# Performance work log

Hardware: AMD Instinct MI355X
Metric: run time of the kernel (lower is better)

## Reference

```python
import jax, jax.numpy as jnp
import numpy as np

B, S, P, D, H, L, DFF = 4, 2048, 32, 512, 8, 2, 2048
HD = D // H
NV = 8  # number of variates; S = NV * 256 patches
SCALE = 1.0 / np.sqrt(HD)


def _rope_tables(seq_len, dim, base=10000.0):
    inv = 1.0 / (base ** (jnp.arange(0, dim, 2, dtype=jnp.float32) / dim))
    freqs = jnp.outer(jnp.arange(seq_len, dtype=jnp.float32), inv)  # (S, dim/2)
    emb = jnp.concatenate([freqs, freqs], axis=-1)  # (S, dim)
    return jnp.cos(emb), jnp.sin(emb)


def _apply_rope(x, cos, sin):
    # x: (..., S, HD); cos/sin: (S, HD)
    x1, x2 = x[..., ::2], x[..., 1::2]
    ch, sh = cos[..., ::2], sin[..., ::2]
    r1 = x1 * ch - x2 * sh
    r2 = x1 * sh + x2 * ch
    return jnp.stack([r1, r2], axis=-1).reshape(x.shape)


def _ln(x, g, b, eps=1e-5):
    m = x.mean(-1, keepdims=True)
    v = x.var(-1, keepdims=True)
    return (x - m) / jnp.sqrt(v + eps) * g + b


def setup_inputs() -> dict:
    key = jax.random.key(0)
    ks = jax.random.split(key, 20)
    s = 0.02
    x = jax.random.normal(ks[0], (B, S, P), dtype=jnp.float32)
    # 8 variates, 256 patches each, flattened: [0]*256, [1]*256, ...
    variate_ids = jnp.broadcast_to(jnp.arange(S, dtype=jnp.int32) // (S // NV), (B, S))
    mask = jnp.ones((B, S), dtype=jnp.float32)
    f32 = jnp.float32
    return {
        'x': x, 'variate_ids': variate_ids, 'mask': mask,
        'W_pe': jax.random.normal(ks[1], (P, D), f32) * s, 'b_pe': jnp.zeros((D,), f32),
        'Wq': jax.random.normal(ks[2], (L, D, D), f32) * s, 'bq': jnp.zeros((L, D), f32),
        'Wk': jax.random.normal(ks[3], (L, D, D), f32) * s, 'bk': jnp.zeros((L, D), f32),
        'Wv': jax.random.normal(ks[4], (L, D, D), f32) * s, 'bv': jnp.zeros((L, D), f32),
        'Wo': jax.random.normal(ks[5], (L, D, D), f32) * s, 'bo': jnp.zeros((L, D), f32),
        'u_same': jax.random.normal(ks[6], (L, H), f32) * 0.1,
        'u_cross': jax.random.normal(ks[7], (L, H), f32) * 0.1,
        'g1': jnp.ones((L, D), f32), 'be1': jnp.zeros((L, D), f32),
        'W1': jax.random.normal(ks[8], (L, D, DFF), f32) * s, 'b1f': jnp.zeros((L, DFF), f32),
        'W2': jax.random.normal(ks[9], (L, DFF, D), f32) * s, 'b2f': jnp.zeros((L, D), f32),
        'g2': jnp.ones((L, D), f32), 'be2': jnp.zeros((L, D), f32),
        'Wh': jax.random.normal(ks[10], (D, P), f32) * s, 'bh': jnp.zeros((P,), f32),
    }


def reference(x, variate_ids, mask, W_pe, b_pe, Wq, bq, Wk, bk, Wv, bv, Wo, bo,
              u_same, u_cross, g1, be1, W1, b1f, W2, b2f, g2, be2, Wh, bh):
    b, s, _ = x.shape
    h = x @ W_pe + b_pe  # patch embedding: (B,S,D)
    cos, sin = _rope_tables(s, HD)
    same = (variate_ids[:, :, None] == variate_ids[:, None, :]).astype(h.dtype)  # (B,S,S)
    mask_add = (1.0 - mask)[:, None, None, :] * -1e9  # (B,1,1,S)
    for l in range(L):
        q = (h @ Wq[l] + bq[l]).reshape(b, s, H, HD).transpose(0, 2, 1, 3)
        k = (h @ Wk[l] + bk[l]).reshape(b, s, H, HD).transpose(0, 2, 1, 3)
        v = (h @ Wv[l] + bv[l]).reshape(b, s, H, HD).transpose(0, 2, 1, 3)
        q = _apply_rope(q, cos, sin)
        k = _apply_rope(k, cos, sin)
        scores = jnp.einsum('bhqd,bhkd->bhqk', q, k) * SCALE
        bias = (same[:, None] * u_same[l][None, :, None, None]
                + (1.0 - same)[:, None] * u_cross[l][None, :, None, None])
        scores = scores + bias + mask_add
        p = jax.nn.softmax(scores, axis=-1)
        o = jnp.einsum('bhqk,bhkd->bhqd', p, v).transpose(0, 2, 1, 3).reshape(b, s, D)
        o = o @ Wo[l] + bo[l]
        h = _ln(h + o, g1[l], be1[l])
        f = jax.nn.gelu(h @ W1[l] + b1f[l], approximate=False) @ W2[l] + b2f[l]
        h = _ln(h + f, g2[l], be2[l])
    return h @ Wh + bh  # forecasting head: (B,S,P)
```

## Files before the change

kernel.cpp:

```cpp
#include <hip/hip_runtime.h>

typedef unsigned short u16;
typedef unsigned int   u32;
typedef __attribute__((ext_vector_type(8))) short bf16x8;
typedef __attribute__((ext_vector_type(4))) short bf16x4;
typedef __attribute__((ext_vector_type(4))) float f32x4;
typedef __attribute__((ext_vector_type(4))) int   i32x4;

constexpr int B_ = 4, S_ = 2048, D_ = 512, H_ = 8, L_ = 2, DFF_ = 2048;
constexpr int BS_ = B_ * S_;
constexpr float QSC_ = 0.18033688011f;
constexpr float LOG2E_ = 1.44269504089f;

__device__ __forceinline__ u16 f2bf(float f) {
    u32 u = __float_as_uint(f);
    u += 0x7fffu + ((u >> 16) & 1u);
    return (u16)(u >> 16);
}
__device__ __forceinline__ float bf2f(u16 u) {
    return __uint_as_float(((u32)u) << 16);
}
__device__ __forceinline__ u32 cvt_pk_bf16(float lo, float hi) {
    u32 d;
    asm volatile("v_cvt_pk_bf16_f32 %0, %1, %2" : "=v"(d) : "v"(lo), "v"(hi));
    return d;
}
__device__ __forceinline__ float exp2v(float x) {
    float d;
    asm("v_exp_f32 %0, %1" : "=v"(d) : "v"(x));
    return d;
}

__global__ __launch_bounds__(256)
void wtrans_all(const float* __restrict__ Wpe, const float* __restrict__ Wq,
                const float* __restrict__ Wk, const float* __restrict__ Wv,
                const float* __restrict__ Wo, const float* __restrict__ W1,
                const float* __restrict__ W2, u16* __restrict__ wpe_t,
                u16* __restrict__ wbase)
{
    __shared__ float tile[32][33];
    int id = blockIdx.x;
    const float* src; u16* dst; int K, N, tx, ty;
    if (id < 16) {
        src = Wpe; dst = wpe_t; K = 32; N = 512; tx = id; ty = 0;
    } else {
        id -= 16;
        if (id < 2048) {
            int mat = id >> 8, l = mat >> 2, w = mat & 3;
            const float* srcs[4] = { Wq, Wk, Wv, Wo };
            src = srcs[w] + (size_t)l * 262144;
            u16* base = wbase + (size_t)l * 3145728;
            dst = base + (size_t)w * 262144;
            K = 512; N = 512;
            int t8 = id & 255; tx = t8 & 15; ty = t8 >> 4;
        } else if (id < 4096) {
            id -= 2048;
            int l = id >> 10, t = id & 1023;
            src = W1 + (size_t)l * 1048576;
            dst = wbase + (size_t)l * 3145728 + 1048576;
            K = 512; N = 2048; tx = t & 63; ty = t >> 6;
        } else {
            id -= 4096;
            int l = id >> 10, t = id & 1023;
            src = W2 + (size_t)l * 1048576;
            dst = wbase + (size_t)l * 3145728 + 2097152;
            K = 2048; N = 512; tx = t & 15; ty = t >> 4;
        }
    }
    const int n0 = tx * 32, k0 = ty * 32;
    const int t = threadIdx.x;
#pragma unroll
    for (int i = 0; i < 4; i++) {
        int lin = i * 256 + t;
        int r = lin >> 5, c = lin & 31;
        tile[r][c] = src[(size_t)(k0 + r) * N + n0 + c];
    }
    __syncthreads();
#pragma unroll
    for (int i = 0; i < 4; i++) {
        int lin = i * 256 + t;
        int r = lin >> 5, c = lin & 31;
        dst[(size_t)(n0 + r) * K + k0 + c] = f2bf(tile[c][r]);
    }
}

__global__ __launch_bounds__(256)
void misc_prep(const float* __restrict__ x, u16* __restrict__ xb,
               const float* __restrict__ bq, const float* __restrict__ bk,
               const float* __restrict__ bv, float* __restrict__ bqkv,
               float* __restrict__ rc, float* __restrict__ rs)
{
    const int id = blockIdx.x, t = threadIdx.x;
    if (id < 256) {
        int idx = id * 256 + t;
        int j = idx & 31, tpos = idx >> 5;
        float inv = __expf(-(float)j * 0.28782313662425572f);
        float ang = (float)tpos * inv;
        rc[idx] = cosf(ang);
        rs[idx] = sinf(ang);
    } else if (id < 512) {
        int i = (id - 256) * 256 + t;
        float4 f = *reinterpret_cast<const float4*>(x + (size_t)i * 4);
        uint2 pk;
        pk.x = (u32)f2bf(f.x) | ((u32)f2bf(f.y) << 16);
        pk.y = (u32)f2bf(f.z) | ((u32)f2bf(f.w) << 16);
        *reinterpret_cast<uint2*>(xb + (size_t)i * 4) = pk;
    } else {
        int idx = (id - 512) * 256 + t;
        if (idx < L_ * 1536) {
            int l = idx / 1536, i = idx % 1536;
            float v = (i < 512) ? bq[l * 512 + i]
                    : (i < 1024) ? bk[l * 512 + i - 512]
                                 : bv[l * 512 + i - 1024];
            bqkv[idx] = v;
        }
    }
}

template<int ACT, int BN, int ROPE>
__global__ __launch_bounds__(256)
void gemm_kernel(const u16* __restrict__ A, const u16* __restrict__ Bt,
                 const float* __restrict__ bias, u16* __restrict__ C,
                 int M, int N, int K, int lda,
                 u16* __restrict__ qd, u16* __restrict__ kd, u16* __restrict__ vd,
                 const float* __restrict__ rc, const float* __restrict__ rs)
{
    constexpr int LDT = 40;
    constexpr int NI = BN / 32;
    __shared__ u16 As[128 * LDT];
    __shared__ u16 Bs[BN * LDT];
    const int t = threadIdx.x;
    const int m0 = blockIdx.y * 128, n0 = blockIdx.x * BN;
    const int lane = t & 63, w = t >> 6;
    const int wr = w >> 1, wc = w & 1;
    const int l15 = lane & 15, lhi = lane >> 4;

    f32x4 acc[4][NI];
#pragma unroll
    for (int i = 0; i < 4; i++)
#pragma unroll
        for (int j = 0; j < NI; j++)
#pragma unroll
            for (int r = 0; r < 4; r++) acc[i][j][r] = 0.f;

    for (int kt = 0; kt < K; kt += 32) {
#pragma unroll
        for (int i = 0; i < 2; i++) {
            int lin = i * 256 + t;
            int r = lin >> 2, c8 = (lin & 3) << 3;
            *reinterpret_cast<bf16x8*>(&As[r * LDT + c8]) =
                *reinterpret_cast<const bf16x8*>(A + (size_t)(m0 + r) * lda + kt + c8);
        }
#pragma unroll
        for (int i = 0; i < BN / 64; i++) {
            int lin = i * 256 + t;
            int r = lin >> 2, c8 = (lin & 3) << 3;
            *reinterpret_cast<bf16x8*>(&Bs[r * LDT + c8]) =
                *reinterpret_cast<const bf16x8*>(Bt + (size_t)(n0 + r) * K + kt + c8);
        }
        __syncthreads();
        bf16x8 af[4], bfv[NI];
#pragma unroll
        for (int mi = 0; mi < 4; mi++)
            af[mi] = *reinterpret_cast<const bf16x8*>(&As[(wr * 64 + mi * 16 + l15) * LDT + lhi * 8]);
#pragma unroll
        for (int ni = 0; ni < NI; ni++)
            bfv[ni] = *reinterpret_cast<const bf16x8*>(&Bs[(wc * (BN / 2) + ni * 16 + l15) * LDT + lhi * 8]);
#pragma unroll
        for (int mi = 0; mi < 4; mi++)
#pragma unroll
            for (int ni = 0; ni < NI; ni++)
                acc[mi][ni] = __builtin_amdgcn_mfma_f32_16x16x32_bf16(af[mi], bfv[ni], acc[mi][ni], 0, 0, 0);
        __syncthreads();
    }

    float bb[NI];
#pragma unroll
    for (int ni = 0; ni < NI; ni++) bb[ni] = bias[n0 + wc * (BN / 2) + ni * 16 + l15];
#pragma unroll
    for (int mi = 0; mi < 4; mi++) {
        int row = m0 + wr * 64 + mi * 16 + lhi * 4;
#pragma unroll
        for (int ni = 0; ni < NI; ni++) {
            int col = n0 + wc * (BN / 2) + ni * 16 + l15;
#pragma unroll
            for (int r = 0; r < 4; r++) {
                float v = acc[mi][ni][r] + bb[ni];
                if (ACT == 1) v = 0.5f * v * (1.0f + erff(v * 0.70710678118654752f));
                C[(size_t)(row + r) * N + col] = f2bf(v);
            }
        }
    }
}

template<int ACT, int BN, int ROPE>
__global__ __launch_bounds__(256)
void gemm_db(const u16* __restrict__ A, const u16* __restrict__ Bt,
             const float* __restrict__ bias, u16* __restrict__ C,
             int M, int N, int K, int lda,
             u16* __restrict__ qd, u16* __restrict__ kd, u16* __restrict__ vd,
             const float* __restrict__ rc, const float* __restrict__ rs)
{
    constexpr int NI = BN / 32;
    constexpr int ABYTES = 128 * 128;
    constexpr int BBYTES = BN * 128;
    constexpr int HALF = ABYTES + BBYTES;
    __shared__ char lds[2 * HALF];
    const int t = threadIdx.x;
    const int m0 = blockIdx.y * 128, n0 = blockIdx.x * BN;
    const int lane = t & 63, w = t >> 6;
    const int wr = w >> 1, wc = w & 1;
    const int l15 = lane & 15, lhi = lane >> 4;
    const int sw = (l15 & 7) << 4;

    auto stage = [&](int kt, int buf) {
        char* base = lds + buf * HALF;
#pragma unroll
        for (int p = 0; p < ABYTES / 4096; p++) {
            int off = p * 4096 + t * 16;
            int so = off ^ (((off >> 7) & 7) << 4);
            int row = off >> 7;
            int col = (so & 127) >> 1;
            __builtin_amdgcn_global_load_lds(
                (const __attribute__((address_space(1))) void*)(A + (size_t)(m0 + row) * lda + kt + col),
                (__attribute__((address_space(3))) void*)(base + off), 16, 0, 0);
        }
        char* bb = base + ABYTES;
#pragma unroll
        for (int p = 0; p < BBYTES / 4096; p++) {
            int off = p * 4096 + t * 16;
            int so = off ^ (((off >> 7) & 7) << 4);
            int row = off >> 7;
            int col = (so & 127) >> 1;
            __builtin_amdgcn_global_load_lds(
                (const __attribute__((address_space(1))) void*)(Bt + (size_t)(n0 + row) * K + kt + col),
                (__attribute__((address_space(3))) void*)(bb + off), 16, 0, 0);
        }
    };

    f32x4 acc[4][NI];
#pragma unroll
    for (int i = 0; i < 4; i++)
#pragma unroll
        for (int j = 0; j < NI; j++)
#pragma unroll
            for (int r = 0; r < 4; r++) acc[i][j][r] = 0.f;

    stage(0, 0);
    int buf = 0;
    for (int kt = 0; kt < K; kt += 64) {
        if (kt + 64 < K) {
            stage(kt + 64, buf ^ 1);
            if constexpr (BN == 64) asm volatile("s_waitcnt vmcnt(6)" ::: "memory");
            else                    asm volatile("s_waitcnt vmcnt(8)" ::: "memory");
        } else {
            asm volatile("s_waitcnt vmcnt(0)" ::: "memory");
        }
        __builtin_amdgcn_s_barrier();
        const char* La = lds + buf * HALF;
        const char* Lb = La + ABYTES;
        bf16x8 af[4][2], bfv[NI][2];
#pragma unroll
        for (int mi = 0; mi < 4; mi++) {
            int row = wr * 64 + mi * 16 + l15;
#pragma unroll
            for (int kk = 0; kk < 2; kk++)
                af[mi][kk] = *reinterpret_cast<const bf16x8*>(La + ((row * 128 + kk * 64 + lhi * 16) ^ sw));
        }
#pragma unroll
        for (int ni = 0; ni < NI; ni++) {
            int row = wc * (BN / 2) + ni * 16 + l15;
#pragma unroll
            for (int kk = 0; kk < 2; kk++)
                bfv[ni][kk] = *reinterpret_cast<const bf16x8*>(Lb + ((row * 128 + kk * 64 + lhi * 16) ^ sw));
        }
        __builtin_amdgcn_s_setprio(1);
#pragma unroll
        for (int kk = 0; kk < 2; kk++)
#pragma unroll
            for (int mi = 0; mi < 4; mi++)
#pragma unroll
                for (int ni = 0; ni < NI; ni++)
                    acc[mi][ni] = __builtin_amdgcn_mfma_f32_16x16x32_bf16(af[mi][kk], bfv[ni][kk], acc[mi][ni], 0, 0, 0);
        __builtin_amdgcn_s_setprio(0);
        __builtin_amdgcn_s_barrier();
        buf ^= 1;
    }

    float bb[NI];
#pragma unroll
    for (int ni = 0; ni < NI; ni++) bb[ni] = bias[n0 + wc * (BN / 2) + ni * 16 + l15];

    if (ROPE == 0) {
#pragma unroll
        for (int mi = 0; mi < 4; mi++) {
            int row = m0 + wr * 64 + mi * 16 + lhi * 4;
#pragma unroll
            for (int ni = 0; ni < NI; ni++) {
                int col = n0 + wc * (BN / 2) + ni * 16 + l15;
#pragma unroll
                for (int r = 0; r < 4; r++) {
                    float v = acc[mi][ni][r] + bb[ni];
                    if (ACT == 1) v = 0.5f * v * (1.0f + erff(v * 0.70710678118654752f));
                    C[(size_t)(row + r) * N + col] = f2bf(v);
                }
            }
        }
    } else {
#pragma unroll
        for (int ni = 0; ni < NI; ni++) {
            int colb = n0 + wc * (BN / 2) + ni * 16;
            int region = colb >> 9;
            int col = colb + l15;
            int d = col & 63;
            int head = (col >> 6) & 7;
#pragma unroll
            for (int mi = 0; mi < 4; mi++) {
                int row0 = m0 + wr * 64 + mi * 16 + lhi * 4;
                int sp0 = row0 & (S_ - 1);
                int bidx0 = row0 >> 11;
                if (region == 2) {
                    float vv[4];
#pragma unroll
                    for (int r = 0; r < 4; r++) vv[r] = acc[mi][ni][r] + bb[ni];
                    uint2 pk;
                    pk.x = (u32)f2bf(vv[0]) | ((u32)f2bf(vv[1]) << 16);
                    pk.y = (u32)f2bf(vv[2]) | ((u32)f2bf(vv[3]) << 16);
                    *reinterpret_cast<uint2*>(vd + (((size_t)(bidx0 * 8 + head) * 64 + d) << 11) + sp0) = pk;
                } else {
#pragma unroll
                    for (int r = 0; r < 4; r++) {
                        int sp = sp0 + r;
                        float v = acc[mi][ni][r] + bb[ni];
                        float px = __shfl_xor(v, 1);
                        int f = d & 30;
                        float cs = rc[sp * 32 + f], sn = rs[sp * 32 + f];
                        float ov = (l15 & 1) ? fmaf(px, sn, v * cs)
                                             : fmaf(v, cs, -(px * sn));
                        if (region == 0) ov *= QSC_;
                        u16* dst = (region == 0) ? qd : kd;
                        dst[((size_t)(bidx0 * 8 + head) * S_ + sp) * 64 + d] = f2bf(ov);
                    }
                }
            }
        }
    }
}

__global__ __launch_bounds__(512, 4)
void attn_kernel(const u16* __restrict__ qbp, const u16* __restrict__ kbp,
                 const u16* __restrict__ vt, const int* __restrict__ vid,
                 const float* __restrict__ maskp,
                 const float* __restrict__ usame, const float* __restrict__ ucross,
                 u16* __restrict__ o)
{
    __shared__ u16 ldsK[3][64 * 64];
    __shared__ u16 ldsV[3][64 * 64];
    __shared__ int   vids[S_];
    __shared__ float madds[S_];
    const int bidx = blockIdx.x;
    const int xcd = bidx & 7;
    const int j = bidx >> 3;
    const int bh = xcd * 4 + (j >> 4);
    const int chunk = j & 15;
    const int b = bh >> 3, hh = bh & 7;
    const int t = threadIdx.x;
    const int lane = t & 63, wid = t >> 6;
    const int q0 = chunk * 128 + wid * 16;
    const int l15 = lane & 15, lhi = lane >> 4;
    const int sw = (l15 & 7) << 4;
    const int ssw = ((t >> 3) & 7) << 4;
    const u16* qp = qbp + (size_t)bh * S_ * 64;
    const u16* kp = kbp + (size_t)bh * S_ * 64;
    const u16* vp = vt + (size_t)bh * 64 * S_;
    const float us = usame[hh] * LOG2E_, uc = ucross[hh] * LOG2E_;
    const int* vidb = vid + (size_t)b * S_;
    const float* mkb = maskp + (size_t)b * S_;
    const bf16x4 ones = { (short)0x3F80, (short)0x3F80, (short)0x3F80, (short)0x3F80 };

    bf16x8 qfr[2];
#pragma unroll
    for (int kk = 0; kk < 2; kk++)
        qfr[kk] = *reinterpret_cast<const bf16x8*>(
            qp + (size_t)(q0 + l15) * 64 + kk * 32 + lhi * 8);

    {
        i32x4 vv = reinterpret_cast<const i32x4*>(vidb)[t];
        f32x4 mm = reinterpret_cast<const f32x4*>(mkb)[t];
        f32x4 md;
#pragma unroll
        for (int r = 0; r < 4; r++) md[r] = (1.0f - mm[r]) * -1.44269504e9f;
        reinterpret_cast<i32x4*>(vids)[t] = vv;
        reinterpret_cast<f32x4*>(madds)[t] = md;
    }

    auto stage = [&](int tile, int buf) {
        const char* kg = (const char*)kp + (size_t)tile * 8192;
        {
            int off = t * 16;
            int so = off ^ ssw;
            __builtin_amdgcn_global_load_lds(
                (const __attribute__((address_space(1))) void*)(kg + so),
                (__attribute__((address_space(3))) void*)((char*)&ldsK[buf][0] + off), 16, 0, 0);
        }
        const char* vg = (const char*)vp + (size_t)tile * 128;
        {
            int off = t * 16;
            int so = off ^ ssw;
            int row = so >> 7, colb = so & 127;
            __builtin_amdgcn_global_load_lds(
                (const __attribute__((address_space(1))) void*)(vg + (size_t)row * 4096 + colb),
                (__attribute__((address_space(3))) void*)((char*)&ldsV[buf][0] + off), 16, 0, 0);
        }
    };

    stage(0, 0);
    stage(1, 1);
    asm volatile("s_waitcnt vmcnt(2) lgkmcnt(0)" ::: "memory");
    __builtin_amdgcn_s_barrier();

    const int vq = vids[q0 + l15];

    float mrow = -1e30f;
    f32x4 lacc;
    f32x4 oT[4];
#pragma unroll
    for (int r = 0; r < 4; r++) lacc[r] = 0.f;
#pragma unroll
    for (int nd = 0; nd < 4; nd++)
#pragma unroll
        for (int r = 0; r < 4; r++) oT[nd][r] = 0.f;

    constexpr int NT = S_ / 64;

    auto qk = [&](int buf, f32x4 (&sx)[4]) {
        const u16* Kb = ldsK[buf];
        __builtin_amdgcn_s_setprio(1);
#pragma unroll
        for (int ni = 0; ni < 4; ni++) {
            int rowb = (ni * 16 + l15) * 128;
            bf16x8 kf0 = *reinterpret_cast<const bf16x8*>((const char*)Kb + ((rowb + lhi * 16) ^ sw));
            bf16x8 kf1 = *reinterpret_cast<const bf16x8*>((const char*)Kb + ((rowb + 64 + lhi * 16) ^ sw));
#pragma unroll
            for (int r = 0; r < 4; r++) sx[ni][r] = 0.f;
            sx[ni] = __builtin_amdgcn_mfma_f32_16x16x32_bf16(kf0, qfr[0], sx[ni], 0, 0, 0);
            sx[ni] = __builtin_amdgcn_mfma_f32_16x16x32_bf16(kf1, qfr[1], sx[ni], 0, 0, 0);
        }
        __builtin_amdgcn_s_setprio(0);
    };

    auto finish = [&](int tt, int buf, f32x4 (&sx)[4]) {
        const int kv0 = tt * 64;
#pragma unroll
        for (int ni = 0; ni < 4; ni++) {
            i32x4 vkq = *reinterpret_cast<const i32x4*>(&vids[kv0 + ni * 16 + lhi * 4]);
            f32x4 md = *reinterpret_cast<const f32x4*>(&madds[kv0 + ni * 16 + lhi * 4]);
#pragma unroll
            for (int r = 0; r < 4; r++)
                sx[ni][r] += (vkq[r] == vq) ? (md[r] + us) : (md[r] + uc);
        }
        float pm = sx[0][0];
#pragma unroll
        for (int ni = 0; ni < 4; ni++)
#pragma unroll
            for (int r = 0; r < 4; r++)
                if (ni || r) pm = fmaxf(pm, sx[ni][r]);
        pm = fmaxf(pm, __shfl_xor(pm, 16));
        pm = fmaxf(pm, __shfl_xor(pm, 32));
        if (!__all(pm <= mrow + 8.f)) {
            float mnew = fmaxf(mrow, pm);
            float alpha = exp2v(mrow - mnew);
            mrow = mnew;
#pragma unroll
            for (int r = 0; r < 4; r++) lacc[r] *= alpha;
#pragma unroll
            for (int nd = 0; nd < 4; nd++)
#pragma unroll
                for (int r = 0; r < 4; r++) oT[nd][r] *= alpha;
        }
        bf16x4 pb[4];
#pragma unroll
        for (int ni = 0; ni < 4; ni++) {
            float p0 = exp2v(sx[ni][0] - mrow);
            float p1 = exp2v(sx[ni][1] - mrow);
            float p2 = exp2v(sx[ni][2] - mrow);
            float p3 = exp2v(sx[ni][3] - mrow);
            union { u32 u[2]; bf16x4 h; } uu;
            uu.u[0] = cvt_pk_bf16(p0, p1);
            uu.u[1] = cvt_pk_bf16(p2, p3);
            pb[ni] = uu.h;
        }
        const u16* Vb = ldsV[buf];
        __builtin_amdgcn_s_setprio(1);
#pragma unroll
        for (int ni = 0; ni < 4; ni++)
            lacc = __builtin_amdgcn_mfma_f32_16x16x16bf16_1k(ones, pb[ni], lacc, 0, 0, 0);
#pragma unroll
        for (int nd = 0; nd < 4; nd++) {
            int rowb = (nd * 16 + l15) * 128;
#pragma unroll
            for (int ni = 0; ni < 4; ni++) {
                bf16x4 vf = *reinterpret_cast<const bf16x4*>((const char*)Vb + ((rowb + ni * 32 + lhi * 8) ^ sw));
                oT[nd] = __builtin_amdgcn_mfma_f32_16x16x16bf16_1k(vf, pb[ni], oT[nd], 0, 0, 0);
            }
        }
        __builtin_amdgcn_s_setprio(0);
    };

    f32x4 s0[4], s1[4];
    qk(0, s0);

    auto step = [&](int u, f32x4 (&sA)[4], f32x4 (&sB)[4]) {
        if (u + 2 < NT) stage(u + 2, (u + 2) % 3);
        if (u + 1 < NT) {
            if (u + 2 < NT) asm volatile("s_waitcnt vmcnt(2)" ::: "memory");
            else            asm volatile("s_waitcnt vmcnt(0)" ::: "memory");
            __builtin_amdgcn_s_barrier();
            qk((u + 1) % 3, sB);
        }
        finish(u, u % 3, sA);
        __builtin_amdgcn_s_barrier();
    };

    for (int tt = 0; tt < NT; tt += 2) {
        step(tt, s0, s1);
        step(tt + 1, s1, s0);
    }

    {
        float inv = 1.0f / lacc[0];
        size_t rowb = (size_t)(b * S_ + q0 + l15) * D_;
#pragma unroll
        for (int nd = 0; nd < 4; nd++) {
            uint2 st;
            st.x = cvt_pk_bf16(oT[nd][0] * inv, oT[nd][1] * inv);
            st.y = cvt_pk_bf16(oT[nd][2] * inv, oT[nd][3] * inv);
            *reinterpret_cast<uint2*>(o + rowb + hh * 64 + nd * 16 + lhi * 4) = st;
        }
    }
}

__global__ __launch_bounds__(256)
void ln_kernel(u16* hb, const u16* __restrict__ tb,
               const float* __restrict__ g, const float* __restrict__ be)
{
    const int row = blockIdx.x * 4 + (threadIdx.x >> 6);
    const int lane = threadIdx.x & 63;
    u16* hp = hb + (size_t)row * D_ + lane * 8;
    const u16* tp = tb + (size_t)row * D_ + lane * 8;
    bf16x8 a = *reinterpret_cast<const bf16x8*>(hp);
    bf16x8 c = *reinterpret_cast<const bf16x8*>(tp);
    float x[8];
    float s = 0.f, s2 = 0.f;
#pragma unroll
    for (int j = 0; j < 8; j++) {
        x[j] = bf2f((u16)a[j]) + bf2f((u16)c[j]);
        s += x[j]; s2 += x[j] * x[j];
    }
#pragma unroll
    for (int m = 1; m <= 32; m <<= 1) { s += __shfl_xor(s, m); s2 += __shfl_xor(s2, m); }
    float mean = s * (1.0f / 512.0f);
    float var = s2 * (1.0f / 512.0f) - mean * mean;
    float rstd = rsqrtf(var + 1e-5f);
    const float* gp = g + lane * 8;
    const float* bp = be + lane * 8;
    bf16x8 ov;
#pragma unroll
    for (int j = 0; j < 8; j++)
        ov[j] = (short)f2bf((x[j] - mean) * rstd * gp[j] + bp[j]);
    *reinterpret_cast<bf16x8*>(hp) = ov;
}

__global__ __launch_bounds__(256)
void head_kernel(const u16* __restrict__ hb, const float* __restrict__ Wh,
                 const float* __restrict__ bhv, float* __restrict__ out)
{
    const int t = threadIdx.x;
    const int p = t & 31, sub = t >> 5;
    const int row = blockIdx.x * 8 + sub;
    const u16* hp = hb + (size_t)row * D_;
    float acc = 0.f;
#pragma unroll 4
    for (int k0 = 0; k0 < D_; k0 += 8) {
        bf16x8 hv = *reinterpret_cast<const bf16x8*>(hp + k0);
#pragma unroll
        for (int j = 0; j < 8; j++)
            acc = fmaf(bf2f((u16)hv[j]), Wh[(size_t)(k0 + j) * 32 + p], acc);
    }
    out[(size_t)row * 32 + p] = acc + bhv[p];
}

extern "C" void kernel_launch(void* const* d_in, const int* in_sizes, int n_in,
                              void* d_out, int out_size, void* d_ws, size_t ws_size,
                              hipStream_t stream)
{
    (void)in_sizes; (void)n_in; (void)out_size; (void)ws_size;
    const float* x     = (const float*)d_in[0];
    const int*   vid   = (const int*)d_in[1];
    const float* maskp = (const float*)d_in[2];
    const float* Wpe   = (const float*)d_in[3];
    const float* bpe   = (const float*)d_in[4];
    const float* Wq    = (const float*)d_in[5];
    const float* bq    = (const float*)d_in[6];
    const float* Wk    = (const float*)d_in[7];
    const float* bk    = (const float*)d_in[8];
    const float* Wv    = (const float*)d_in[9];
    const float* bv    = (const float*)d_in[10];
    const float* Wo    = (const float*)d_in[11];
    const float* bo    = (const float*)d_in[12];
    const float* usame = (const float*)d_in[13];
    const float* ucros = (const float*)d_in[14];
    const float* g1    = (const float*)d_in[15];
    const float* be1   = (const float*)d_in[16];
    const float* W1    = (const float*)d_in[17];
    const float* b1f   = (const float*)d_in[18];
    const float* W2    = (const float*)d_in[19];
    const float* b2f   = (const float*)d_in[20];
    const float* g2    = (const float*)d_in[21];
    const float* be2   = (const float*)d_in[22];
    const float* Whd   = (const float*)d_in[23];
    const float* bhd   = (const float*)d_in[24];

    constexpr size_t MB = 1024ull * 1024ull;
    char* ws = (char*)d_ws;
    u16*   hb   = (u16*)(ws + 0);
    u16*   qbb  = (u16*)(ws + 8 * MB);
    u16*   kbb  = (u16*)(ws + 16 * MB);
    u16*   vtb  = (u16*)(ws + 24 * MB);
    u16*   ob   = (u16*)(ws + 40 * MB);
    u16*   tb   = (u16*)(ws + 48 * MB);
    u16*   fb   = (u16*)(ws + 56 * MB);
    u16*   xb   = (u16*)(ws + 88 * MB);
    float* rc   = (float*)(ws + 89 * MB);
    float* rs   = (float*)(ws + 89 * MB + 262144);
    float* bqkv = (float*)(ws + 90 * MB);
    u16*   wpe_t = (u16*)(ws + 91 * MB);
    u16*   wbase = (u16*)(ws + 92 * MB);

    auto qkvt = [&](int l) { return wbase + (size_t)l * 3145728; };
    auto wot  = [&](int l) { return qkvt(l) + 786432; };
    auto w1t  = [&](int l) { return qkvt(l) + 1048576; };
    auto w2t  = [&](int l) { return qkvt(l) + 2097152; };

    wtrans_all<<<6160, 256, 0, stream>>>(Wpe, Wq, Wk, Wv, Wo, W1, W2, wpe_t, wbase);
    misc_prep<<<524, 256, 0, stream>>>(x, xb, bq, bk, bv, bqkv, rc, rs);

    gemm_kernel<0, 64, 0><<<dim3(8, 64), 256, 0, stream>>>(
        xb, wpe_t, bpe, hb, BS_, 512, 32, 32,
        (u16*)nullptr, (u16*)nullptr, (u16*)nullptr, (const float*)nullptr, (const float*)nullptr);

    for (int l = 0; l < L_; l++) {
        gemm_db<0, 128, 1><<<dim3(12, 64), 256, 0, stream>>>(
            hb, qkvt(l), bqkv + l * 1536, (u16*)nullptr, BS_, 1536, 512, 512,
            qbb, kbb, vtb, rc, rs);
        attn_kernel<<<512, 512, 0, stream>>>(qbb, kbb, vtb, vid, maskp,
                                             usame + l * H_, ucros + l * H_, ob);
        gemm_db<0, 64, 0><<<dim3(8, 64), 256, 0, stream>>>(
            ob, wot(l), bo + l * 512, tb, BS_, 512, 512, 512,
            (u16*)nullptr, (u16*)nullptr, (u16*)nullptr, (const float*)nullptr, (const float*)nullptr);
        ln_kernel<<<2048, 256, 0, stream>>>(hb, tb, g1 + l * 512, be1 + l * 512);
        gemm_db<1, 128, 0><<<dim3(16, 64), 256, 0, stream>>>(
            hb, w1t(l), b1f + l * 2048, fb, BS_, 2048, 512, 512,
            (u16*)nullptr, (u16*)nullptr, (u16*)nullptr, (const float*)nullptr, (const float*)nullptr);
        gemm_db<0, 64, 0><<<dim3(8, 64), 256, 0, stream>>>(
            fb, w2t(l), b2f + l * 512, tb, BS_, 512, 2048, 2048,
            (u16*)nullptr, (u16*)nullptr, (u16*)nullptr, (const float*)nullptr, (const float*)nullptr);
        ln_kernel<<<2048, 256, 0, stream>>>(hb, tb, g2 + l * 512, be2 + l * 512);
    }
    head_kernel<<<1024, 256, 0, stream>>>(hb, Whd, bhd, (float*)d_out);
}
```

Before: 413.0 us.

## Use MFMA head GEMM, fold attention bias into accumulator init, widen N tiles

```diff
diff --git a/kernel.cpp b/kernel.cpp
--- a/kernel.cpp
+++ b/kernel.cpp
@@ -35,7 +35,8 @@
 void wtrans_all(const float* __restrict__ Wpe, const float* __restrict__ Wq,
                 const float* __restrict__ Wk, const float* __restrict__ Wv,
                 const float* __restrict__ Wo, const float* __restrict__ W1,
-                const float* __restrict__ W2, u16* __restrict__ wpe_t,
+                const float* __restrict__ W2, const float* __restrict__ Whd,
+                u16* __restrict__ wpe_t, u16* __restrict__ whd_t,
                 u16* __restrict__ wbase)
 {
     __shared__ float tile[32][33];
@@ -43,6 +44,8 @@
     const float* src; u16* dst; int K, N, tx, ty;
     if (id < 16) {
         src = Wpe; dst = wpe_t; K = 32; N = 512; tx = id; ty = 0;
+    } else if (id >= 6160) {
+        src = Whd; dst = whd_t; K = 512; N = 32; tx = 0; ty = id - 6160;
     } else {
         id -= 16;
         if (id < 2048) {
@@ -357,7 +360,7 @@
     __shared__ u16 ldsK[3][64 * 64];
     __shared__ u16 ldsV[3][64 * 64];
     __shared__ int   vids[S_];
-    __shared__ float madds[S_];
+    __shared__ float cbase[S_];
     const int bidx = blockIdx.x;
     const int xcd = bidx & 7;
     const int j = bidx >> 3;
@@ -374,6 +377,7 @@
     const u16* kp = kbp + (size_t)bh * S_ * 64;
     const u16* vp = vt + (size_t)bh * 64 * S_;
     const float us = usame[hh] * LOG2E_, uc = ucross[hh] * LOG2E_;
+    const float df = us - uc;
     const int* vidb = vid + (size_t)b * S_;
     const float* mkb = maskp + (size_t)b * S_;
     const bf16x4 ones = { (short)0x3F80, (short)0x3F80, (short)0x3F80, (short)0x3F80 };
@@ -387,11 +391,11 @@
     {
         i32x4 vv = reinterpret_cast<const i32x4*>(vidb)[t];
         f32x4 mm = reinterpret_cast<const f32x4*>(mkb)[t];
-        f32x4 md;
-#pragma unroll
-        for (int r = 0; r < 4; r++) md[r] = (1.0f - mm[r]) * -1.44269504e9f;
+        f32x4 cb;
+#pragma unroll
+        for (int r = 0; r < 4; r++) cb[r] = fmaf(1.0f - mm[r], -1.44269504e9f, uc);
         reinterpret_cast<i32x4*>(vids)[t] = vv;
-        reinterpret_cast<f32x4*>(madds)[t] = md;
+        reinterpret_cast<f32x4*>(cbase)[t] = cb;
     }
 
     auto stage = [&](int tile, int buf) {
@@ -433,17 +437,17 @@
 
     constexpr int NT = S_ / 64;
 
-    auto qk = [&](int buf, f32x4 (&sx)[4]) {
+    auto qk = [&](int buf, int tile, f32x4 (&sx)[4]) {
         const u16* Kb = ldsK[buf];
+        const int kv0 = tile * 64;
         __builtin_amdgcn_s_setprio(1);
 #pragma unroll
         for (int ni = 0; ni < 4; ni++) {
+            f32x4 cb = *reinterpret_cast<const f32x4*>(&cbase[kv0 + ni * 16 + lhi * 4]);
             int rowb = (ni * 16 + l15) * 128;
             bf16x8 kf0 = *reinterpret_cast<const bf16x8*>((const char*)Kb + ((rowb + lhi * 16) ^ sw));
             bf16x8 kf1 = *reinterpret_cast<const bf16x8*>((const char*)Kb + ((rowb + 64 + lhi * 16) ^ sw));
-#pragma unroll
-            for (int r = 0; r < 4; r++) sx[ni][r] = 0.f;
-            sx[ni] = __builtin_amdgcn_mfma_f32_16x16x32_bf16(kf0, qfr[0], sx[ni], 0, 0, 0);
+            sx[ni] = __builtin_amdgcn_mfma_f32_16x16x32_bf16(kf0, qfr[0], cb, 0, 0, 0);
             sx[ni] = __builtin_amdgcn_mfma_f32_16x16x32_bf16(kf1, qfr[1], sx[ni], 0, 0, 0);
         }
         __builtin_amdgcn_s_setprio(0);
@@ -454,10 +458,9 @@
 #pragma unroll
         for (int ni = 0; ni < 4; ni++) {
             i32x4 vkq = *reinterpret_cast<const i32x4*>(&vids[kv0 + ni * 16 + lhi * 4]);
-            f32x4 md = *reinterpret_cast<const f32x4*>(&madds[kv0 + ni * 16 + lhi * 4]);
 #pragma unroll
             for (int r = 0; r < 4; r++)
-                sx[ni][r] += (vkq[r] == vq) ? (md[r] + us) : (md[r] + uc);
+                sx[ni][r] += (vkq[r] == vq) ? df : 0.f;
         }
         float pm = sx[0][0];
 #pragma unroll
@@ -508,7 +511,7 @@
     };
 
     f32x4 s0[4], s1[4];
-    qk(0, s0);
+    qk(0, 0, s0);
 
     auto step = [&](int u, f32x4 (&sA)[4], f32x4 (&sB)[4]) {
         if (u + 2 < NT) stage(u + 2, (u + 2) % 3);
@@ -516,7 +519,7 @@
             if (u + 2 < NT) asm volatile("s_waitcnt vmcnt(2)" ::: "memory");
             else            asm volatile("s_waitcnt vmcnt(0)" ::: "memory");
             __builtin_amdgcn_s_barrier();
-            qk((u + 1) % 3, sB);
+            qk((u + 1) % 3, u + 1, sB);
         }
         finish(u, u % 3, sA);
         __builtin_amdgcn_s_barrier();
@@ -572,22 +575,57 @@
 }
 
 __global__ __launch_bounds__(256)
-void head_kernel(const u16* __restrict__ hb, const float* __restrict__ Wh,
-                 const float* __restrict__ bhv, float* __restrict__ out)
+void head_mfma(const u16* __restrict__ hb, const u16* __restrict__ wht,
+               const float* __restrict__ bhv, float* __restrict__ out)
 {
+    __shared__ u16 Bs[32 * 520];
     const int t = threadIdx.x;
-    const int p = t & 31, sub = t >> 5;
-    const int row = blockIdx.x * 8 + sub;
-    const u16* hp = hb + (size_t)row * D_;
-    float acc = 0.f;
+#pragma unroll
+    for (int i = 0; i < 8; i++) {
+        int idx = i * 256 + t;
+        int n = idx >> 6, kc = idx & 63;
+        *reinterpret_cast<bf16x8*>(&Bs[n * 520 + kc * 8]) =
+            reinterpret_cast<const bf16x8*>(wht)[idx];
+    }
+    __syncthreads();
+    const int lane = t & 63, w = t >> 6;
+    const int l15 = lane & 15, lhi = lane >> 4;
+    const int row0 = blockIdx.x * 128 + w * 32;
+
+    f32x4 acc[2][2];
+#pragma unroll
+    for (int mi = 0; mi < 2; mi++)
+#pragma unroll
+        for (int ni = 0; ni < 2; ni++)
+#pragma unroll
+            for (int r = 0; r < 4; r++) acc[mi][ni][r] = 0.f;
+
 #pragma unroll 4
-    for (int k0 = 0; k0 < D_; k0 += 8) {
-        bf16x8 hv = *reinterpret_cast<const bf16x8*>(hp + k0);
-#pragma unroll
-        for (int j = 0; j < 8; j++)
-            acc = fmaf(bf2f((u16)hv[j]), Wh[(size_t)(k0 + j) * 32 + p], acc);
-    }
-    out[(size_t)row * 32 + p] = acc + bhv[p];
+    for (int kt = 0; kt < 512; kt += 32) {
+        bf16x8 af[2], bf[2];
+#pragma unroll
+        for (int mi = 0; mi < 2; mi++)
+            af[mi] = *reinterpret_cast<const bf16x8*>(
+                hb + (size_t)(row0 + mi * 16 + l15) * 512 + kt + lhi * 8);
+#pragma unroll
+        for (int ni = 0; ni < 2; ni++)
+            bf[ni] = *reinterpret_cast<const bf16x8*>(&Bs[(ni * 16 + l15) * 520 + kt + lhi * 8]);
+#pragma unroll
+        for (int mi = 0; mi < 2; mi++)
+#pragma unroll
+            for (int ni = 0; ni < 2; ni++)
+                acc[mi][ni] = __builtin_amdgcn_mfma_f32_16x16x32_bf16(af[mi], bf[ni], acc[mi][ni], 0, 0, 0);
+    }
+#pragma unroll
+    for (int mi = 0; mi < 2; mi++)
+#pragma unroll
+        for (int ni = 0; ni < 2; ni++) {
+            int col = ni * 16 + l15;
+            float bv = bhv[col];
+#pragma unroll
+            for (int r = 0; r < 4; r++)
+                out[(size_t)(row0 + mi * 16 + lhi * 4 + r) * 32 + col] = acc[mi][ni][r] + bv;
+        }
 }
 
 extern "C" void kernel_launch(void* const* d_in, const int* in_sizes, int n_in,
@@ -635,6 +673,7 @@
     float* rs   = (float*)(ws + 89 * MB + 262144);
     float* bqkv = (float*)(ws + 90 * MB);
     u16*   wpe_t = (u16*)(ws + 91 * MB);
+    u16*   whd_t = (u16*)(ws + 91 * MB + 65536);
     u16*   wbase = (u16*)(ws + 92 * MB);
 
     auto qkvt = [&](int l) { return wbase + (size_t)l * 3145728; };
@@ -642,7 +681,8 @@
     auto w1t  = [&](int l) { return qkvt(l) + 1048576; };
     auto w2t  = [&](int l) { return qkvt(l) + 2097152; };
 
-    wtrans_all<<<6160, 256, 0, stream>>>(Wpe, Wq, Wk, Wv, Wo, W1, W2, wpe_t, wbase);
+    wtrans_all<<<6176, 256, 0, stream>>>(Wpe, Wq, Wk, Wv, Wo, W1, W2, Whd,
+                                         wpe_t, whd_t, wbase);
     misc_prep<<<524, 256, 0, stream>>>(x, xb, bq, bk, bv, bqkv, rc, rs);
 
     gemm_kernel<0, 64, 0><<<dim3(8, 64), 256, 0, stream>>>(
@@ -655,17 +695,17 @@
             qbb, kbb, vtb, rc, rs);
         attn_kernel<<<512, 512, 0, stream>>>(qbb, kbb, vtb, vid, maskp,
                                              usame + l * H_, ucros + l * H_, ob);
-        gemm_db<0, 64, 0><<<dim3(8, 64), 256, 0, stream>>>(
+        gemm_db<0, 128, 0><<<dim3(4, 64), 256, 0, stream>>>(
             ob, wot(l), bo + l * 512, tb, BS_, 512, 512, 512,
             (u16*)nullptr, (u16*)nullptr, (u16*)nullptr, (const float*)nullptr, (const float*)nullptr);
         ln_kernel<<<2048, 256, 0, stream>>>(hb, tb, g1 + l * 512, be1 + l * 512);
         gemm_db<1, 128, 0><<<dim3(16, 64), 256, 0, stream>>>(
             hb, w1t(l), b1f + l * 2048, fb, BS_, 2048, 512, 512,
             (u16*)nullptr, (u16*)nullptr, (u16*)nullptr, (const float*)nullptr, (const float*)nullptr);
-        gemm_db<0, 64, 0><<<dim3(8, 64), 256, 0, stream>>>(
+        gemm_db<0, 128, 0><<<dim3(4, 64), 256, 0, stream>>>(
             fb, w2t(l), b2f + l * 512, tb, BS_, 512, 2048, 2048,
             (u16*)nullptr, (u16*)nullptr, (u16*)nullptr, (const float*)nullptr, (const float*)nullptr);
         ln_kernel<<<2048, 256, 0, stream>>>(hb, tb, g2 + l * 512, be2 + l * 512);
     }
-    head_kernel<<<1024, 256, 0, stream>>>(hb, Whd, bhd, (float*)d_out);
-}
+    head_mfma<<<64, 256, 0, stream>>>(hb, whd_t, bhd, (float*)d_out);
+}
```

Measured after the change: 357.2 us. -13.5%, faster.
